# Optimization experiments

Measured on AMD Instinct MI355X. Metric: run time of the kernel, lower is better.

Reference implementation:

```python
import jax, jax.numpy as jnp
import numpy as np

B, N, D_IN, D_OUT, HEADS = 4, 4096, 1024, 1024, 16
D_HEAD = D_OUT // HEADS  # scale_factor in the torch module


def setup_inputs() -> dict:
    key = jax.random.key(0)
    ks = jax.random.split(key, 5)
    x = jax.random.normal(ks[0], (B, N, D_IN), dtype=jnp.float32)
    s_in = 1.0 / np.sqrt(D_IN)
    s_out = 1.0 / np.sqrt(D_OUT)
    Wq = jax.random.normal(ks[1], (D_IN, D_OUT), dtype=jnp.float32) * s_in
    Wk = jax.random.normal(ks[2], (D_IN, D_OUT), dtype=jnp.float32) * s_in
    Wv = jax.random.normal(ks[3], (D_IN, D_OUT), dtype=jnp.float32) * s_in
    Wo = jax.random.normal(ks[4], (D_OUT, D_OUT), dtype=jnp.float32) * s_out
    bo = jnp.zeros((D_OUT,), dtype=jnp.float32)
    return {"x": x, "Wq": Wq, "Wk": Wk, "Wv": Wv, "Wo": Wo, "bo": bo}


def reference(x, Wq, Wk, Wv, Wo, bo):
    # Linear attention (Efficient Attention): softmax(Q, feat) @ (softmax(K, seq)^T @ V)
    q = jax.nn.softmax(jnp.einsum('bni,io->bno', x, Wq), axis=-1)   # [B,N,D] softmax over features
    k = jax.nn.softmax(jnp.einsum('bni,io->bno', x, Wk), axis=-2)   # [B,N,D] softmax over sequence
    v = jnp.einsum('bni,io->bno', x, Wv)                             # [B,N,D]
    scale = 1.0 / np.sqrt(D_HEAD).astype(np.float32)
    # context = K^T V : [B, D, D] -- avoids the [B, N, N] score matrix
    ctx = jnp.einsum('bnd,bne->bde', k, v) * scale
    y = jnp.einsum('bnd,bde->bne', q, ctx) / jnp.float32(D_OUT)      # final per-elem / shape[-1]
    # dropout is identity in eval mode
    return jnp.einsum('bnd,de->bne', y, Wo) + bo
```

## Files before the change

### kernel.cpp

```cpp
#include <hip/hip_runtime.h>

typedef _Float16 half_t;
typedef __attribute__((ext_vector_type(8))) _Float16 half8;
typedef __attribute__((ext_vector_type(4))) _Float16 half4;
typedef __attribute__((ext_vector_type(4))) float f32x4;

#define B_ 4
#define N_ 4096
#define D_ 1024
#define R_ (B_ * N_)

__device__ __forceinline__ void gload_lds16(const half_t* g, half_t* l) {
    __builtin_amdgcn_global_load_lds(
        (const __attribute__((address_space(1))) unsigned int*)g,
        (__attribute__((address_space(3))) unsigned int*)l, 16, 0, 0);
}

__device__ __forceinline__ void wgbar() {
    asm volatile("" ::: "memory");
    __builtin_amdgcn_s_barrier();
    asm volatile("" ::: "memory");
}

template <int EPI, int ZSHIFT, int SWAP>
__global__ __launch_bounds__(512, 2) void gemm256(
    const half_t* __restrict__ A, const half_t* __restrict__ Bt,
    void* __restrict__ Cv, const float* __restrict__ bias,
    int lda, int ldb, int ldc, int K,
    long sA, long sB, long sC, float scale)
{
    __shared__ __align__(16) half_t As[2][2][256 * 32];
    __shared__ __align__(16) half_t Bs[2][2][256 * 32];

    const int t = threadIdx.x;
    const int wave = t >> 6;
    const int lane = t & 63;
    const int l15 = lane & 15;
    const int q = lane >> 4;
    const int wm = wave >> 2;
    const int wn = wave & 3;
    const int m0 = (SWAP ? blockIdx.x : blockIdx.y) * 256;
    const int n0 = (SWAP ? blockIdx.y : blockIdx.x) * 256;
    const long zb = blockIdx.z >> ZSHIFT;
    const int zs = blockIdx.z & ((1 << ZSHIFT) - 1);

    const int c0 = t, c1 = t + 512;
    const int r0 = c0 >> 2, r1 = c1 >> 2;
    const int g0 = ((c0 & 3) ^ ((c0 >> 3) & 3)) * 8;
    const int g1 = ((c1 & 3) ^ ((c1 >> 3) & 3)) * 8;

    const half_t* Ab = A + zb * sA + (long)m0 * lda + zs * K;
    const half_t* Bb = Bt + zb * sB + (long)n0 * ldb + zs * K;
    const long a0 = (long)r0 * lda + g0, a1 = (long)r1 * lda + g1;
    const long b0 = (long)r0 * ldb + g0, b1 = (long)r1 * ldb + g1;

    const int qq = (q ^ ((l15 >> 1) & 3)) * 8;

    f32x4 acc[8][4] = {};
    const int nk2 = K >> 6;

#define STAGE_A(tt, ks) do { const int kb_ = (tt) * 64 + (ks) * 32; \
        gload_lds16(Ab + a0 + kb_, &As[(tt) & 1][ks][c0 * 8]);      \
        gload_lds16(Ab + a1 + kb_, &As[(tt) & 1][ks][c1 * 8]); } while (0)
#define STAGE_B(tt, ks) do { const int kb_ = (tt) * 64 + (ks) * 32; \
        gload_lds16(Bb + b0 + kb_, &Bs[(tt) & 1][ks][c0 * 8]);      \
        gload_lds16(Bb + b1 + kb_, &Bs[(tt) & 1][ks][c1 * 8]); } while (0)
#define LDB4(ksb) _Pragma("unroll") \
    for (int j = 0; j < 4; j++)     \
        bf[j] = *(const half8*)&Bs[cur][ksb][(wn * 64 + j * 16 + l15) * 32 + qq];
#define LDA4(ksb, mh) _Pragma("unroll") \
    for (int i = 0; i < 4; i++)         \
        af[i] = *(const half8*)&As[cur][ksb][(wm * 128 + (mh) * 64 + i * 16 + l15) * 32 + qq];
#define MFMA16(ar) _Pragma("unroll")                    \
    for (int i = 0; i < 4; i++) _Pragma("unroll")       \
        for (int j = 0; j < 4; j++)                     \
            acc[(ar) + i][j] = __builtin_amdgcn_mfma_f32_16x16x32_f16(af[i], bf[j], acc[(ar) + i][j], 0, 0, 0);

    STAGE_A(0, 0); STAGE_B(0, 0); STAGE_A(0, 1); STAGE_B(0, 1);
    if (nk2 > 1) {
        STAGE_A(1, 0); STAGE_B(1, 0); STAGE_B(1, 1);
        asm volatile("s_waitcnt vmcnt(6)" ::: "memory");
    } else {
        asm volatile("s_waitcnt vmcnt(0)" ::: "memory");
    }
    wgbar();

    for (int tt = 0; tt < nk2; ++tt) {
        const int cur = tt & 1;
        half8 af[4], bf[4];
        LDB4(0); LDA4(0, 0);
        if (tt + 1 < nk2) STAGE_A(tt + 1, 1);
        wgbar();
        __builtin_amdgcn_s_setprio(1); MFMA16(0); __builtin_amdgcn_s_setprio(0);
        wgbar();
        LDA4(0, 1);
        if (tt + 2 < nk2) STAGE_B(tt + 2, 0);
        wgbar();
        __builtin_amdgcn_s_setprio(1); MFMA16(4); __builtin_amdgcn_s_setprio(0);
        wgbar();
        LDB4(1); LDA4(1, 0);
        if (tt + 2 < nk2) STAGE_A(tt + 2, 0);
        wgbar();
        __builtin_amdgcn_s_setprio(1); MFMA16(0); __builtin_amdgcn_s_setprio(0);
        wgbar();
        LDA4(1, 1);
        if (tt + 2 < nk2) STAGE_B(tt + 2, 1);
        wgbar();
        __builtin_amdgcn_s_setprio(1); MFMA16(4); __builtin_amdgcn_s_setprio(0);
        if (tt + 2 < nk2) asm volatile("s_waitcnt vmcnt(6)" ::: "memory");
        else              asm volatile("s_waitcnt vmcnt(0)" ::: "memory");
        wgbar();
    }
#undef STAGE_A
#undef STAGE_B
#undef LDB4
#undef LDA4
#undef MFMA16

    if (EPI == 1) {
        half_t* C = (half_t*)Cv + (long)blockIdx.z * sC + (long)m0 * ldc + n0;
#pragma unroll
        for (int a = 0; a < 8; a++) {
            const int rowb = wm * 128 + (a >> 2) * 64 + (a & 3) * 16 + q * 4;
#pragma unroll
            for (int j = 0; j < 4; j++) {
                const int col = wn * 64 + j * 16 + l15;
#pragma unroll
                for (int r = 0; r < 4; r++)
                    C[(long)(rowb + r) * ldc + col] = (half_t)(acc[a][j][r] * scale);
            }
        }
    } else {
        float* C = (float*)Cv + (long)blockIdx.z * sC + (long)m0 * ldc + n0;
#pragma unroll
        for (int a = 0; a < 8; a++) {
            const int rowb = wm * 128 + (a >> 2) * 64 + (a & 3) * 16 + q * 4;
#pragma unroll
            for (int j = 0; j < 4; j++) {
                const int col = wn * 64 + j * 16 + l15;
                const float bv = (EPI == 2) ? bias[n0 + col] : 0.0f;
#pragma unroll
                for (int r = 0; r < 4; r++)
                    C[(long)(rowb + r) * ldc + col] = acc[a][j][r] * scale + bv;
            }
        }
    }
}

__global__ __launch_bounds__(256) void ctx_reduce_h(
    const half_t* __restrict__ P, half_t* __restrict__ ctx)
{
    const long i = ((long)blockIdx.x * 256 + threadIdx.x) * 8;
    const long b = i >> 20;
    const long idx = i & ((1L << 20) - 1);
    const half_t* p = P + (b * 4) * (1L << 20) + idx;
    const half8 s0 = *(const half8*)(p);
    const half8 s1 = *(const half8*)(p + (1L << 20));
    const half8 s2 = *(const half8*)(p + 2 * (1L << 20));
    const half8 s3 = *(const half8*)(p + 3 * (1L << 20));
    half8 o;
#pragma unroll
    for (int j = 0; j < 8; j++)
        o[j] = (half_t)((float)s0[j] + (float)s1[j] + (float)s2[j] + (float)s3[j]);
    *(half8*)(ctx + i) = o;
}

__global__ __launch_bounds__(256) void prep_fused(
    const float* __restrict__ x,
    const float* __restrict__ W0, const float* __restrict__ W1,
    const float* __restrict__ W2, const float* __restrict__ W3,
    half_t* __restrict__ Wt, half_t* __restrict__ Wvh, half_t* __restrict__ Xh)
{
    const int bid = blockIdx.x;
    const int t = threadIdx.x;
    if (bid < 4096) {
        __shared__ float tile[32][33];
        const int z = bid >> 10;
        const int rem = bid & 1023;
        const int by = (rem >> 5) * 32, bx = (rem & 31) * 32;
        const float* W = z == 0 ? W0 : z == 1 ? W1 : z == 2 ? W2 : W3;
        half_t* dst = Wt + (size_t)z * 1024 * 1024;
        const int tx = t & 31, ty = t >> 5;
#pragma unroll
        for (int yy = ty; yy < 32; yy += 8)
            tile[yy][tx] = W[(long)(by + yy) * 1024 + bx + tx];
        __syncthreads();
#pragma unroll
        for (int yy = ty; yy < 32; yy += 8)
            dst[(long)(bx + yy) * 1024 + by + tx] = (half_t)tile[tx][yy];
    } else if (bid < 4608) {
        const long i = ((long)(bid - 4096) * 256 + t) * 8;
        const float4 a = *(const float4*)(W2 + i);
        const float4 b = *(const float4*)(W2 + i + 4);
        half8 o = {(half_t)a.x, (half_t)a.y, (half_t)a.z, (half_t)a.w,
                   (half_t)b.x, (half_t)b.y, (half_t)b.z, (half_t)b.w};
        *(half8*)(Wvh + i) = o;
    } else {
        const long i = ((long)(bid - 4608) * 256 + t) * 8;
        const float4 a = *(const float4*)(x + i);
        const float4 b = *(const float4*)(x + i + 4);
        half8 o = {(half_t)a.x, (half_t)a.y, (half_t)a.z, (half_t)a.w,
                   (half_t)b.x, (half_t)b.y, (half_t)b.z, (half_t)b.w};
        *(half8*)(Xh + i) = o;
    }
}

__global__ __launch_bounds__(256) void softmax_fused(
    const half_t* __restrict__ KV, half_t* __restrict__ Kt,
    const half_t* __restrict__ Qlog, half_t* __restrict__ Qh)
{
    const int bid = blockIdx.x;
    const int t = threadIdx.x;
    if (bid < B_ * D_) {
        const long r = bid;
        const long b = r >> 10;
        const long d = r & 1023;
        const half_t* row = KV + (b * 2048 + d) * 4096;
        const half8 h0 = *(const half8*)(row + t * 16);
        const half8 h1 = *(const half8*)(row + t * 16 + 8);
        float v[16];
#pragma unroll
        for (int j = 0; j < 8; j++) { v[j] = (float)h0[j]; v[8 + j] = (float)h1[j]; }
        float m = v[0];
#pragma unroll
        for (int j = 1; j < 16; j++) m = fmaxf(m, v[j]);
#pragma unroll
        for (int o = 32; o > 0; o >>= 1) m = fmaxf(m, __shfl_xor(m, o, 64));
        __shared__ float redm[4], reds[4];
        const int wave = t >> 6;
        if ((t & 63) == 0) redm[wave] = m;
        __syncthreads();
        m = fmaxf(fmaxf(redm[0], redm[1]), fmaxf(redm[2], redm[3]));
        float s = 0.0f;
#pragma unroll
        for (int j = 0; j < 16; j++) { v[j] = __expf(v[j] - m); s += v[j]; }
#pragma unroll
        for (int o = 32; o > 0; o >>= 1) s += __shfl_xor(s, o, 64);
        if ((t & 63) == 0) reds[wave] = s;
        __syncthreads();
        s = reds[0] + reds[1] + reds[2] + reds[3];
        const float rs = 64.0f / s;
        half8 o0, o1;
#pragma unroll
        for (int j = 0; j < 8; j++) {
            o0[j] = (half_t)(v[j] * rs);
            o1[j] = (half_t)(v[8 + j] * rs);
        }
        *(half8*)(Kt + r * 4096 + t * 16) = o0;
        *(half8*)(Kt + r * 4096 + t * 16 + 8) = o1;
    } else {
        const long r = ((long)(bid - B_ * D_)) * 4 + (t >> 6);
        const int lane = t & 63;
        const half_t* row = Qlog + r * 1024 + lane * 16;
        const half8 h0 = *(const half8*)(row);
        const half8 h1 = *(const half8*)(row + 8);
        float v[16];
#pragma unroll
        for (int j = 0; j < 8; j++) { v[j] = (float)h0[j]; v[8 + j] = (float)h1[j]; }
        float m = v[0];
#pragma unroll
        for (int j = 1; j < 16; j++) m = fmaxf(m, v[j]);
#pragma unroll
        for (int o = 32; o > 0; o >>= 1) m = fmaxf(m, __shfl_xor(m, o, 64));
        float s = 0.0f;
#pragma unroll
        for (int j = 0; j < 16; j++) { v[j] = __expf(v[j] - m); s += v[j]; }
#pragma unroll
        for (int o = 32; o > 0; o >>= 1) s += __shfl_xor(s, o, 64);
        const float rs = 64.0f / s;
        half8 o0, o1;
#pragma unroll
        for (int j = 0; j < 8; j++) {
            o0[j] = (half_t)(v[j] * rs);
            o1[j] = (half_t)(v[8 + j] * rs);
        }
        half_t* orow = Qh + r * 1024 + lane * 16;
        *(half8*)(orow) = o0;
        *(half8*)(orow + 8) = o1;
    }
}

extern "C" void kernel_launch(void* const* d_in, const int* in_sizes, int n_in,
                              void* d_out, int out_size, void* d_ws, size_t ws_size,
                              hipStream_t stream)
{
    const float* x  = (const float*)d_in[0];
    const float* Wq = (const float*)d_in[1];
    const float* Wk = (const float*)d_in[2];
    const float* Wv = (const float*)d_in[3];
    const float* Wo = (const float*)d_in[4];
    const float* bo = (const float*)d_in[5];
    float* out = (float*)d_out;

    char* w = (char*)d_ws;
    half_t* Xh  = (half_t*)w;
    half_t* P   = (half_t*)w;
    w += (size_t)R_ * D_ * 2;
    half_t* KVreg = (half_t*)w;
    w += (size_t)B_ * 2048 * 4096 * 2;
    half_t* Qh  = (half_t*)w; w += (size_t)R_ * D_ * 2;
    half_t* Kt  = (half_t*)w; w += (size_t)R_ * D_ * 2;
    half_t* Pw  = Kt;
    half_t* Wt  = (half_t*)w; w += (size_t)4 * D_ * D_ * 2;
    half_t* ctxT = (half_t*)w; w += (size_t)B_ * D_ * D_ * 2;
    half_t* Wvh = (half_t*)w; w += (size_t)B_ * D_ * D_ * 2;
    half_t* Qlog = (half_t*)out;
    (void)ws_size; (void)in_sizes; (void)n_in; (void)out_size;

    const dim3 blk(256);
    const dim3 blkg(512);
    const long M1 = 1L << 20;

    prep_fused<<<12800, blk, 0, stream>>>(x, Wq, Wk, Wv, Wo, Wt, Wvh, Xh);

    gemm256<1, 2, 1><<<dim3(4, 4, 4), blkg, 0, stream>>>(Wt + 3 * M1, Wvh, Pw, nullptr,
        1024, 1024, 1024, 256, 0, 0, M1, 1.0f);
    ctx_reduce_h<<<512, blk, 0, stream>>>(Pw, Wt + 2 * M1);

    gemm256<1, 0, 1><<<dim3(64, 4, 1), blkg, 0, stream>>>(Xh, Wt, Qlog, nullptr,
        1024, 1024, 1024, 1024, 0, 0, 0, 1.0f);

    gemm256<1, 0, 0><<<dim3(16, 8, B_), blkg, 0, stream>>>(Wt + M1, Xh, KVreg, nullptr,
        1024, 1024, 4096, 1024, 0, (long)N_ * D_, (long)2048 * 4096, 1.0f);

    softmax_fused<<<B_ * D_ + R_ / 4, blk, 0, stream>>>(KVreg, Kt, Qlog, Qh);

    gemm256<1, 2, 1><<<dim3(4, 4, 16), blkg, 0, stream>>>(KVreg + (long)1024 * 4096, Kt, P, nullptr,
        4096, 4096, 1024, N_ / 4,
        (long)2048 * 4096, (long)D_ * N_, M1, 1.0f);
    ctx_reduce_h<<<2048, blk, 0, stream>>>(P, ctxT);

    gemm256<2, 0, 1><<<dim3(16, 4, B_), blkg, 0, stream>>>(Qh, ctxT, out, bo,
        1024, 1024, 1024, 1024,
        (long)N_ * D_, M1, (long)N_ * D_,
        1.0f / 33554432.0f);
}
```

Baseline: 364.7 us.

## Shrink GEMM tiles to 128x256 with simpler double-buffered K loop for occupancy

Replaces the 256x256 GEMM with a 128x256 tile kernel that stages a 32-wide K slice per iteration into a double buffer. This halves accumulators and LDS use so four workgroups can fit per CU, and doubles the grid size of every GEMM launch. The elaborate split-phase pipeline with interleaved barriers is dropped for a single wait-and-barrier per K step. Smaller tiles lower operand reuse and raise global and LDS traffic, and the simpler schedule may expose load latency.

```diff
diff --git a/kernel.cpp b/kernel.cpp
--- a/kernel.cpp
+++ b/kernel.cpp
@@ -23,14 +23,14 @@
 }
 
 template <int EPI, int ZSHIFT, int SWAP>
-__global__ __launch_bounds__(512, 2) void gemm256(
+__global__ __launch_bounds__(512, 4) void gemmco(
     const half_t* __restrict__ A, const half_t* __restrict__ Bt,
     void* __restrict__ Cv, const float* __restrict__ bias,
     int lda, int ldb, int ldc, int K,
     long sA, long sB, long sC, float scale)
 {
-    __shared__ __align__(16) half_t As[2][2][256 * 32];
-    __shared__ __align__(16) half_t Bs[2][2][256 * 32];
+    __shared__ __align__(16) half_t As[2][128 * 32];
+    __shared__ __align__(16) half_t Bs[2][256 * 32];
 
     const int t = threadIdx.x;
     const int wave = t >> 6;
@@ -39,109 +39,86 @@
     const int q = lane >> 4;
     const int wm = wave >> 2;
     const int wn = wave & 3;
-    const int m0 = (SWAP ? blockIdx.x : blockIdx.y) * 256;
+    const int m0 = (SWAP ? blockIdx.x : blockIdx.y) * 128;
     const int n0 = (SWAP ? blockIdx.y : blockIdx.x) * 256;
     const long zb = blockIdx.z >> ZSHIFT;
     const int zs = blockIdx.z & ((1 << ZSHIFT) - 1);
 
     const int c0 = t, c1 = t + 512;
-    const int r0 = c0 >> 2, r1 = c1 >> 2;
-    const int g0 = ((c0 & 3) ^ ((c0 >> 3) & 3)) * 8;
-    const int g1 = ((c1 & 3) ^ ((c1 >> 3) & 3)) * 8;
+    const int gA = ((c0 & 3) ^ ((c0 >> 3) & 3)) * 8;
+    const int gB1 = ((c1 & 3) ^ ((c1 >> 3) & 3)) * 8;
+    const int rA = c0 >> 2;
+    const int rB1 = c1 >> 2;
 
     const half_t* Ab = A + zb * sA + (long)m0 * lda + zs * K;
     const half_t* Bb = Bt + zb * sB + (long)n0 * ldb + zs * K;
-    const long a0 = (long)r0 * lda + g0, a1 = (long)r1 * lda + g1;
-    const long b0 = (long)r0 * ldb + g0, b1 = (long)r1 * ldb + g1;
+    const long a0 = (long)rA * lda + gA;
+    const long b0 = (long)rA * ldb + gA;
+    const long b1 = (long)rB1 * ldb + gB1;
 
     const int qq = (q ^ ((l15 >> 1) & 3)) * 8;
 
-    f32x4 acc[8][4] = {};
-    const int nk2 = K >> 6;
-
-#define STAGE_A(tt, ks) do { const int kb_ = (tt) * 64 + (ks) * 32; \
-        gload_lds16(Ab + a0 + kb_, &As[(tt) & 1][ks][c0 * 8]);      \
-        gload_lds16(Ab + a1 + kb_, &As[(tt) & 1][ks][c1 * 8]); } while (0)
-#define STAGE_B(tt, ks) do { const int kb_ = (tt) * 64 + (ks) * 32; \
-        gload_lds16(Bb + b0 + kb_, &Bs[(tt) & 1][ks][c0 * 8]);      \
-        gload_lds16(Bb + b1 + kb_, &Bs[(tt) & 1][ks][c1 * 8]); } while (0)
-#define LDB4(ksb) _Pragma("unroll") \
-    for (int j = 0; j < 4; j++)     \
-        bf[j] = *(const half8*)&Bs[cur][ksb][(wn * 64 + j * 16 + l15) * 32 + qq];
-#define LDA4(ksb, mh) _Pragma("unroll") \
-    for (int i = 0; i < 4; i++)         \
-        af[i] = *(const half8*)&As[cur][ksb][(wm * 128 + (mh) * 64 + i * 16 + l15) * 32 + qq];
-#define MFMA16(ar) _Pragma("unroll")                    \
-    for (int i = 0; i < 4; i++) _Pragma("unroll")       \
-        for (int j = 0; j < 4; j++)                     \
-            acc[(ar) + i][j] = __builtin_amdgcn_mfma_f32_16x16x32_f16(af[i], bf[j], acc[(ar) + i][j], 0, 0, 0);
-
-    STAGE_A(0, 0); STAGE_B(0, 0); STAGE_A(0, 1); STAGE_B(0, 1);
-    if (nk2 > 1) {
-        STAGE_A(1, 0); STAGE_B(1, 0); STAGE_B(1, 1);
-        asm volatile("s_waitcnt vmcnt(6)" ::: "memory");
-    } else {
-        asm volatile("s_waitcnt vmcnt(0)" ::: "memory");
+    f32x4 acc[4][4] = {};
+    const int nk = K >> 5;
+
+#define STAGE(kt) do { const int kb_ = (kt) * 32; const int bf_ = (kt) & 1; \
+        gload_lds16(Ab + a0 + kb_, &As[bf_][c0 * 8]);                       \
+        gload_lds16(Bb + b0 + kb_, &Bs[bf_][c0 * 8]);                       \
+        gload_lds16(Bb + b1 + kb_, &Bs[bf_][c1 * 8]); } while (0)
+
+    STAGE(0);
+    asm volatile("s_waitcnt vmcnt(0)" ::: "memory");
+    wgbar();
+
+    for (int kt = 0; kt < nk; ++kt) {
+        const int cur = kt & 1;
+        if (kt + 1 < nk) STAGE(kt + 1);
+        half8 af[4], bf[4];
+#pragma unroll
+        for (int j = 0; j < 4; j++)
+            bf[j] = *(const half8*)&Bs[cur][(wn * 64 + j * 16 + l15) * 32 + qq];
+#pragma unroll
+        for (int i = 0; i < 4; i++)
+            af[i] = *(const half8*)&As[cur][(wm * 64 + i * 16 + l15) * 32 + qq];
+        __builtin_amdgcn_s_setprio(1);
+#pragma unroll
+        for (int i = 0; i < 4; i++)
+#pragma unroll
+            for (int j = 0; j < 4; j++)
+                acc[i][j] = __builtin_amdgcn_mfma_f32_16x16x32_f16(af[i], bf[j], acc[i][j], 0, 0, 0);
+        __builtin_amdgcn_s_setprio(0);
+        if (kt + 1 < nk) {
+            asm volatile("s_waitcnt vmcnt(0)" ::: "memory");
+            wgbar();
+        }
     }
-    wgbar();
-
-    for (int tt = 0; tt < nk2; ++tt) {
-        const int cur = tt & 1;
-        half8 af[4], bf[4];
-        LDB4(0); LDA4(0, 0);
-        if (tt + 1 < nk2) STAGE_A(tt + 1, 1);
-        wgbar();
-        __builtin_amdgcn_s_setprio(1); MFMA16(0); __builtin_amdgcn_s_setprio(0);
-        wgbar();
-        LDA4(0, 1);
-        if (tt + 2 < nk2) STAGE_B(tt + 2, 0);
-        wgbar();
-        __builtin_amdgcn_s_setprio(1); MFMA16(4); __builtin_amdgcn_s_setprio(0);
-        wgbar();
-        LDB4(1); LDA4(1, 0);
-        if (tt + 2 < nk2) STAGE_A(tt + 2, 0);
-        wgbar();
-        __builtin_amdgcn_s_setprio(1); MFMA16(0); __builtin_amdgcn_s_setprio(0);
-        wgbar();
-        LDA4(1, 1);
-        if (tt + 2 < nk2) STAGE_B(tt + 2, 1);
-        wgbar();
-        __builtin_amdgcn_s_setprio(1); MFMA16(4); __builtin_amdgcn_s_setprio(0);
-        if (tt + 2 < nk2) asm volatile("s_waitcnt vmcnt(6)" ::: "memory");
-        else              asm volatile("s_waitcnt vmcnt(0)" ::: "memory");
-        wgbar();
-    }
-#undef STAGE_A
-#undef STAGE_B
-#undef LDB4
-#undef LDA4
-#undef MFMA16
+#undef STAGE
 
     if (EPI == 1) {
         half_t* C = (half_t*)Cv + (long)blockIdx.z * sC + (long)m0 * ldc + n0;
 #pragma unroll
-        for (int a = 0; a < 8; a++) {
-            const int rowb = wm * 128 + (a >> 2) * 64 + (a & 3) * 16 + q * 4;
+        for (int i = 0; i < 4; i++) {
+            const int rowb = wm * 64 + i * 16 + q * 4;
 #pragma unroll
             for (int j = 0; j < 4; j++) {
                 const int col = wn * 64 + j * 16 + l15;
 #pragma unroll
                 for (int r = 0; r < 4; r++)
-                    C[(long)(rowb + r) * ldc + col] = (half_t)(acc[a][j][r] * scale);
+                    C[(long)(rowb + r) * ldc + col] = (half_t)(acc[i][j][r] * scale);
             }
         }
     } else {
         float* C = (float*)Cv + (long)blockIdx.z * sC + (long)m0 * ldc + n0;
 #pragma unroll
-        for (int a = 0; a < 8; a++) {
-            const int rowb = wm * 128 + (a >> 2) * 64 + (a & 3) * 16 + q * 4;
+        for (int i = 0; i < 4; i++) {
+            const int rowb = wm * 64 + i * 16 + q * 4;
 #pragma unroll
             for (int j = 0; j < 4; j++) {
                 const int col = wn * 64 + j * 16 + l15;
                 const float bv = (EPI == 2) ? bias[n0 + col] : 0.0f;
 #pragma unroll
                 for (int r = 0; r < 4; r++)
-                    C[(long)(rowb + r) * ldc + col] = acc[a][j][r] * scale + bv;
+                    C[(long)(rowb + r) * ldc + col] = acc[i][j][r] * scale + bv;
             }
         }
     }
@@ -313,24 +290,24 @@
 
     prep_fused<<<12800, blk, 0, stream>>>(x, Wq, Wk, Wv, Wo, Wt, Wvh, Xh);
 
-    gemm256<1, 2, 1><<<dim3(4, 4, 4), blkg, 0, stream>>>(Wt + 3 * M1, Wvh, Pw, nullptr,
+    gemmco<1, 2, 1><<<dim3(8, 4, 4), blkg, 0, stream>>>(Wt + 3 * M1, Wvh, Pw, nullptr,
         1024, 1024, 1024, 256, 0, 0, M1, 1.0f);
     ctx_reduce_h<<<512, blk, 0, stream>>>(Pw, Wt + 2 * M1);
 
-    gemm256<1, 0, 1><<<dim3(64, 4, 1), blkg, 0, stream>>>(Xh, Wt, Qlog, nullptr,
+    gemmco<1, 0, 1><<<dim3(128, 4, 1), blkg, 0, stream>>>(Xh, Wt, Qlog, nullptr,
         1024, 1024, 1024, 1024, 0, 0, 0, 1.0f);
 
-    gemm256<1, 0, 0><<<dim3(16, 8, B_), blkg, 0, stream>>>(Wt + M1, Xh, KVreg, nullptr,
+    gemmco<1, 0, 0><<<dim3(16, 16, B_), blkg, 0, stream>>>(Wt + M1, Xh, KVreg, nullptr,
         1024, 1024, 4096, 1024, 0, (long)N_ * D_, (long)2048 * 4096, 1.0f);
 
     softmax_fused<<<B_ * D_ + R_ / 4, blk, 0, stream>>>(KVreg, Kt, Qlog, Qh);
 
-    gemm256<1, 2, 1><<<dim3(4, 4, 16), blkg, 0, stream>>>(KVreg + (long)1024 * 4096, Kt, P, nullptr,
+    gemmco<1, 2, 1><<<dim3(8, 4, 16), blkg, 0, stream>>>(KVreg + (long)1024 * 4096, Kt, P, nullptr,
         4096, 4096, 1024, N_ / 4,
         (long)2048 * 4096, (long)D_ * N_, M1, 1.0f);
     ctx_reduce_h<<<2048, blk, 0, stream>>>(P, ctxT);
 
-    gemm256<2, 0, 1><<<dim3(16, 4, B_), blkg, 0, stream>>>(Qh, ctxT, out, bo,
+    gemmco<2, 0, 1><<<dim3(32, 4, B_), blkg, 0, stream>>>(Qh, ctxT, out, bo,
         1024, 1024, 1024, 1024,
         (long)N_ * D_, M1, (long)N_ * D_,
         1.0f / 33554432.0f);
```

Result: slower. 382.8 us (+5.0%).

## Load one GEMM operand directly into registers, stage only the other via LDS

Applied to the files above, without the earlier changes.

Adds two GEMM variants that stream one operand (B in gemmrgB, A in gemmrgA) straight from global memory into registers with a two-deep register prefetch. Only the other operand goes through a triple-buffered LDS ring. Four of the five gemm256 launches now use these variants, while the K^T V launch stays on gemm256. The aim is to cut LDS traffic, LDS footprint and barrier pressure. The trade-off is more VGPRs, non-shared per-wave global loads that may duplicate traffic across waves, and hand-tuned vmcnt waits that must match the load counts exactly.

```diff
diff --git a/kernel.cpp b/kernel.cpp
--- a/kernel.cpp
+++ b/kernel.cpp
@@ -20,6 +20,232 @@
     asm volatile("" ::: "memory");
     __builtin_amdgcn_s_barrier();
     asm volatile("" ::: "memory");
+}
+
+
+template <int EPI, int ZSHIFT, int SWAP>
+__global__ __launch_bounds__(512, 2) void gemmrgB(
+    const half_t* __restrict__ A, const half_t* __restrict__ Bt,
+    void* __restrict__ Cv, const float* __restrict__ bias,
+    int lda, int ldb, int ldc, int K,
+    long sA, long sB, long sC, float scale)
+{
+    __shared__ __align__(16) half_t As[3][256 * 32];
+
+    const int t = threadIdx.x;
+    const int wave = t >> 6;
+    const int lane = t & 63;
+    const int l15 = lane & 15;
+    const int q = lane >> 4;
+    const int wm = wave >> 2;
+    const int wn = wave & 3;
+    const int m0 = (SWAP ? blockIdx.x : blockIdx.y) * 256;
+    const int n0 = (SWAP ? blockIdx.y : blockIdx.x) * 256;
+    const long zb = blockIdx.z >> ZSHIFT;
+    const int zs = blockIdx.z & ((1 << ZSHIFT) - 1);
+
+    const int c0 = t, c1 = t + 512;
+    const int g0 = ((c0 & 3) ^ ((c0 >> 3) & 3)) * 8;
+    const int g1 = ((c1 & 3) ^ ((c1 >> 3) & 3)) * 8;
+    const half_t* Ab = A + zb * sA + (long)m0 * lda + zs * K;
+    const long a0 = (long)(c0 >> 2) * lda + g0;
+    const long a1 = (long)(c1 >> 2) * lda + g1;
+
+    const half_t* Bb = Bt + zb * sB + (long)n0 * ldb + zs * K + q * 8;
+    const half_t* bgl0 = Bb + (long)(wn * 64 +  0 + l15) * ldb;
+    const half_t* bgl1 = Bb + (long)(wn * 64 + 16 + l15) * ldb;
+    const half_t* bgl2 = Bb + (long)(wn * 64 + 32 + l15) * ldb;
+    const half_t* bgl3 = Bb + (long)(wn * 64 + 48 + l15) * ldb;
+
+    const int qq = (q ^ ((l15 >> 1) & 3)) * 8;
+
+    f32x4 acc[8][4] = {};
+    const int nk = K >> 5;
+    half8 bf0[4], bf1[4];
+
+#define STAGE_A(kt) do { const int kb_ = (kt) * 32; half_t* d_ = As[(kt) % 3]; \
+        gload_lds16(Ab + a0 + kb_, d_ + c0 * 8);                               \
+        gload_lds16(Ab + a1 + kb_, d_ + c1 * 8); } while (0)
+#define BLOAD(kt, bfv) do { const long ko_ = (long)(kt) * 32;                  \
+        asm volatile("global_load_dwordx4 %0, %1, off" : "=v"(bfv[0]) : "v"(bgl0 + ko_)); \
+        asm volatile("global_load_dwordx4 %0, %1, off" : "=v"(bfv[1]) : "v"(bgl1 + ko_)); \
+        asm volatile("global_load_dwordx4 %0, %1, off" : "=v"(bfv[2]) : "v"(bgl2 + ko_)); \
+        asm volatile("global_load_dwordx4 %0, %1, off" : "=v"(bfv[3]) : "v"(bgl3 + ko_)); \
+    } while (0)
+#define TILE(kt, BFC, BFN) do {                                                \
+    if ((kt) + 2 < nk) STAGE_A((kt) + 2);                                      \
+    half8 af[8];                                                               \
+    _Pragma("unroll") for (int i = 0; i < 8; i++)                              \
+        af[i] = *(const half8*)&As[(kt) % 3][(wm * 128 + i * 16 + l15) * 32 + qq]; \
+    __builtin_amdgcn_s_setprio(1);                                             \
+    _Pragma("unroll") for (int i = 0; i < 8; i++)                              \
+    _Pragma("unroll") for (int j = 0; j < 4; j++)                              \
+        acc[i][j] = __builtin_amdgcn_mfma_f32_16x16x32_f16(af[i], BFC[j], acc[i][j], 0, 0, 0); \
+    __builtin_amdgcn_s_setprio(0);                                             \
+    if ((kt) + 2 < nk) BLOAD((kt) + 2, BFC);                                   \
+    if ((kt) + 2 < nk)      asm volatile("s_waitcnt vmcnt(6)" ::: "memory");   \
+    else if ((kt) + 1 < nk) asm volatile("s_waitcnt vmcnt(0)" ::: "memory");   \
+    __builtin_amdgcn_sched_barrier(0);                                         \
+    if ((kt) + 1 < nk) wgbar();                                                \
+    __builtin_amdgcn_sched_barrier(0);                                         \
+} while (0)
+
+    STAGE_A(0); BLOAD(0, bf0);
+    STAGE_A(1); BLOAD(1, bf1);
+    asm volatile("s_waitcnt vmcnt(6)" ::: "memory");
+    __builtin_amdgcn_sched_barrier(0);
+    wgbar();
+    __builtin_amdgcn_sched_barrier(0);
+
+    for (int tt = 0; tt < nk; tt += 2) {
+        TILE(tt, bf0, bf1);
+        TILE(tt + 1, bf1, bf0);
+    }
+#undef STAGE_A
+#undef BLOAD
+#undef TILE
+
+    if (EPI == 1) {
+        half_t* C = (half_t*)Cv + (long)blockIdx.z * sC + (long)m0 * ldc + n0;
+#pragma unroll
+        for (int i = 0; i < 8; i++) {
+            const int rowb = wm * 128 + i * 16 + q * 4;
+#pragma unroll
+            for (int j = 0; j < 4; j++) {
+                const int col = wn * 64 + j * 16 + l15;
+#pragma unroll
+                for (int r = 0; r < 4; r++)
+                    C[(long)(rowb + r) * ldc + col] = (half_t)(acc[i][j][r] * scale);
+            }
+        }
+    } else {
+        float* C = (float*)Cv + (long)blockIdx.z * sC + (long)m0 * ldc + n0;
+#pragma unroll
+        for (int i = 0; i < 8; i++) {
+            const int rowb = wm * 128 + i * 16 + q * 4;
+#pragma unroll
+            for (int j = 0; j < 4; j++) {
+                const int col = wn * 64 + j * 16 + l15;
+                const float bv = (EPI == 2) ? bias[n0 + col] : 0.0f;
+#pragma unroll
+                for (int r = 0; r < 4; r++)
+                    C[(long)(rowb + r) * ldc + col] = acc[i][j][r] * scale + bv;
+            }
+        }
+    }
+}
+
+template <int EPI, int ZSHIFT, int SWAP>
+__global__ __launch_bounds__(512, 2) void gemmrgA(
+    const half_t* __restrict__ A, const half_t* __restrict__ Bt,
+    void* __restrict__ Cv, const float* __restrict__ bias,
+    int lda, int ldb, int ldc, int K,
+    long sA, long sB, long sC, float scale)
+{
+    __shared__ __align__(16) half_t Bs[3][256 * 32];
+
+    const int t = threadIdx.x;
+    const int wave = t >> 6;
+    const int lane = t & 63;
+    const int l15 = lane & 15;
+    const int q = lane >> 4;
+    const int wm = wave >> 2;
+    const int wn = wave & 3;
+    const int m0 = (SWAP ? blockIdx.x : blockIdx.y) * 256;
+    const int n0 = (SWAP ? blockIdx.y : blockIdx.x) * 256;
+    const long zb = blockIdx.z >> ZSHIFT;
+    const int zs = blockIdx.z & ((1 << ZSHIFT) - 1);
+
+    const int c0 = t, c1 = t + 512;
+    const int g0 = ((c0 & 3) ^ ((c0 >> 3) & 3)) * 8;
+    const int g1 = ((c1 & 3) ^ ((c1 >> 3) & 3)) * 8;
+    const half_t* Bb = Bt + zb * sB + (long)n0 * ldb + zs * K;
+    const long b0 = (long)(c0 >> 2) * ldb + g0;
+    const long b1 = (long)(c1 >> 2) * ldb + g1;
+
+    const half_t* apb = A + zb * sA + (long)(m0 + wm * 128 + l15) * lda + zs * K + q * 8;
+    const long rstep = 16 * (long)lda;
+
+    const int qq = (q ^ ((l15 >> 1) & 3)) * 8;
+
+    f32x4 acc[8][4] = {};
+    const int nk = K >> 5;
+    half8 af0[8], af1[8];
+
+#define STAGE_B(kt) do { const int kb_ = (kt) * 32; half_t* d_ = Bs[(kt) % 3]; \
+        gload_lds16(Bb + b0 + kb_, d_ + c0 * 8);                               \
+        gload_lds16(Bb + b1 + kb_, d_ + c1 * 8); } while (0)
+#define ALOAD(kt, afv) do { const long ko_ = (long)(kt) * 32;                  \
+        asm volatile("global_load_dwordx4 %0, %1, off" : "=v"(afv[0]) : "v"(apb + 0 * rstep + ko_)); \
+        asm volatile("global_load_dwordx4 %0, %1, off" : "=v"(afv[1]) : "v"(apb + 1 * rstep + ko_)); \
+        asm volatile("global_load_dwordx4 %0, %1, off" : "=v"(afv[2]) : "v"(apb + 2 * rstep + ko_)); \
+        asm volatile("global_load_dwordx4 %0, %1, off" : "=v"(afv[3]) : "v"(apb + 3 * rstep + ko_)); \
+        asm volatile("global_load_dwordx4 %0, %1, off" : "=v"(afv[4]) : "v"(apb + 4 * rstep + ko_)); \
+        asm volatile("global_load_dwordx4 %0, %1, off" : "=v"(afv[5]) : "v"(apb + 5 * rstep + ko_)); \
+        asm volatile("global_load_dwordx4 %0, %1, off" : "=v"(afv[6]) : "v"(apb + 6 * rstep + ko_)); \
+        asm volatile("global_load_dwordx4 %0, %1, off" : "=v"(afv[7]) : "v"(apb + 7 * rstep + ko_)); \
+    } while (0)
+#define TILEA(kt, AFC, AFN) do {                                               \
+    if ((kt) + 2 < nk) STAGE_B((kt) + 2);                                      \
+    half8 bf[4];                                                               \
+    _Pragma("unroll") for (int j = 0; j < 4; j++)                              \
+        bf[j] = *(const half8*)&Bs[(kt) % 3][(wn * 64 + j * 16 + l15) * 32 + qq]; \
+    __builtin_amdgcn_s_setprio(1);                                             \
+    _Pragma("unroll") for (int i = 0; i < 8; i++)                              \
+    _Pragma("unroll") for (int j = 0; j < 4; j++)                              \
+        acc[i][j] = __builtin_amdgcn_mfma_f32_16x16x32_f16(AFC[i], bf[j], acc[i][j], 0, 0, 0); \
+    __builtin_amdgcn_s_setprio(0);                                             \
+    if ((kt) + 2 < nk) ALOAD((kt) + 2, AFC);                                   \
+    if ((kt) + 2 < nk)      asm volatile("s_waitcnt vmcnt(10)" ::: "memory");  \
+    else if ((kt) + 1 < nk) asm volatile("s_waitcnt vmcnt(0)" ::: "memory");   \
+    __builtin_amdgcn_sched_barrier(0);                                         \
+    if ((kt) + 1 < nk) wgbar();                                                \
+    __builtin_amdgcn_sched_barrier(0);                                         \
+} while (0)
+
+    STAGE_B(0); ALOAD(0, af0);
+    STAGE_B(1); ALOAD(1, af1);
+    asm volatile("s_waitcnt vmcnt(10)" ::: "memory");
+    __builtin_amdgcn_sched_barrier(0);
+    wgbar();
+    __builtin_amdgcn_sched_barrier(0);
+
+    for (int tt = 0; tt < nk; tt += 2) {
+        TILEA(tt, af0, af1);
+        TILEA(tt + 1, af1, af0);
+    }
+#undef STAGE_B
+#undef ALOAD
+#undef TILEA
+
+    if (EPI == 1) {
+        half_t* C = (half_t*)Cv + (long)blockIdx.z * sC + (long)m0 * ldc + n0;
+#pragma unroll
+        for (int i = 0; i < 8; i++) {
+            const int rowb = wm * 128 + i * 16 + q * 4;
+#pragma unroll
+            for (int j = 0; j < 4; j++) {
+                const int col = wn * 64 + j * 16 + l15;
+#pragma unroll
+                for (int r = 0; r < 4; r++)
+                    C[(long)(rowb + r) * ldc + col] = (half_t)(acc[i][j][r] * scale);
+            }
+        }
+    } else {
+        float* C = (float*)Cv + (long)blockIdx.z * sC + (long)m0 * ldc + n0;
+#pragma unroll
+        for (int i = 0; i < 8; i++) {
+            const int rowb = wm * 128 + i * 16 + q * 4;
+#pragma unroll
+            for (int j = 0; j < 4; j++) {
+                const int col = wn * 64 + j * 16 + l15;
+                const float bv = (EPI == 2) ? bias[n0 + col] : 0.0f;
+#pragma unroll
+                for (int r = 0; r < 4; r++)
+                    C[(long)(rowb + r) * ldc + col] = acc[i][j][r] * scale + bv;
+            }
+        }
+    }
 }
 
 template <int EPI, int ZSHIFT, int SWAP>
@@ -313,14 +539,14 @@
 
     prep_fused<<<12800, blk, 0, stream>>>(x, Wq, Wk, Wv, Wo, Wt, Wvh, Xh);
 
-    gemm256<1, 2, 1><<<dim3(4, 4, 4), blkg, 0, stream>>>(Wt + 3 * M1, Wvh, Pw, nullptr,
+    gemmrgB<1, 2, 1><<<dim3(4, 4, 4), blkg, 0, stream>>>(Wt + 3 * M1, Wvh, Pw, nullptr,
         1024, 1024, 1024, 256, 0, 0, M1, 1.0f);
     ctx_reduce_h<<<512, blk, 0, stream>>>(Pw, Wt + 2 * M1);
 
-    gemm256<1, 0, 1><<<dim3(64, 4, 1), blkg, 0, stream>>>(Xh, Wt, Qlog, nullptr,
+    gemmrgB<1, 0, 1><<<dim3(64, 4, 1), blkg, 0, stream>>>(Xh, Wt, Qlog, nullptr,
         1024, 1024, 1024, 1024, 0, 0, 0, 1.0f);
 
-    gemm256<1, 0, 0><<<dim3(16, 8, B_), blkg, 0, stream>>>(Wt + M1, Xh, KVreg, nullptr,
+    gemmrgA<1, 0, 0><<<dim3(16, 8, B_), blkg, 0, stream>>>(Wt + M1, Xh, KVreg, nullptr,
         1024, 1024, 4096, 1024, 0, (long)N_ * D_, (long)2048 * 4096, 1.0f);
 
     softmax_fused<<<B_ * D_ + R_ / 4, blk, 0, stream>>>(KVreg, Kt, Qlog, Qh);
@@ -330,7 +556,7 @@
         (long)2048 * 4096, (long)D_ * N_, M1, 1.0f);
     ctx_reduce_h<<<2048, blk, 0, stream>>>(P, ctxT);
 
-    gemm256<2, 0, 1><<<dim3(16, 4, B_), blkg, 0, stream>>>(Qh, ctxT, out, bo,
+    gemmrgB<2, 0, 1><<<dim3(16, 4, B_), blkg, 0, stream>>>(Qh, ctxT, out, bo,
         1024, 1024, 1024, 1024,
         (long)N_ * D_, M1, (long)N_ * D_,
         1.0f / 33554432.0f);
```

Measured after the change: 457.3 us. 25.4% more time.
